# Kernel optimization log

Hardware: AMD Instinct MI355X
Metric: run time of the kernel (lower is better)

Reference implementation:

```python
import jax, jax.numpy as jnp
import numpy as np

NUM_DAYS = 4096
NUM_ATTR = 512
MB = 128  # minibatch_size (sliding-window length)
HID = 500


def setup_inputs() -> dict:
    key = jax.random.key(0)
    kx, k1, kb1, k2, kb2 = jax.random.split(key, 5)
    bound1 = 1.0 / np.sqrt(NUM_ATTR)
    bound2 = 1.0 / np.sqrt(HID)
    return {
        "x": jax.random.normal(kx, (NUM_DAYS, NUM_ATTR), dtype=jnp.float32),
        "W1": jax.random.uniform(k1, (NUM_ATTR, HID), jnp.float32, -bound1, bound1),
        "b1": jax.random.uniform(kb1, (HID,), jnp.float32, -bound1, bound1),
        "W2": jax.random.uniform(k2, (HID, 1), jnp.float32, -bound2, bound2),
        "b2": jax.random.uniform(kb2, (1,), jnp.float32, -bound2, bound2),
    }


def reference(x, W1, b1, W2, b2):
    num_days = x.shape[0]
    num_batches = num_days - MB  # number of sliding windows
    # window gather indices: [num_batches, MB]
    idx = jnp.arange(num_batches)[:, None] + jnp.arange(MB)[None, :]
    xw = x[idx]                                   # [num_batches, MB, num_attr]
    h = jnp.einsum('wma,ah->wmh', xw, W1) + b1    # [num_batches, MB, 500]
    out = jnp.einsum('wmh,ho->wmo', h, W2) + b2   # [num_batches, MB, 1]
    # torch loop cats all windows along dim 0 (first window replaces sentinel)
    return out.reshape(num_batches * MB, 1)
```

## Files before the change

kernel.cpp:

```cpp
#include <hip/hip_runtime.h>

#define NUM_DAYS   4096
#define NUM_ATTR   512
#define MB_WIN     128
#define HID        500
#define NUM_BATCHES (NUM_DAYS - MB_WIN)
#define NUM_Y       (NUM_BATCHES + MB_WIN - 1)
#define OUT_ELEMS   (NUM_BATCHES * MB_WIN)

__global__ __launch_bounds__(64) void k_fold_weights(
    const float* __restrict__ W1, const float* __restrict__ b1,
    const float* __restrict__ W2, const float* __restrict__ b2,
    float* __restrict__ v, float* __restrict__ c) {
    const int b    = blockIdx.x;
    const int lane = threadIdx.x;
    float acc = 0.f;
    if (b < NUM_ATTR) {
        const float* row = W1 + (size_t)b * HID;
        for (int h = lane; h < HID; h += 64) acc += row[h] * W2[h];
    } else {
        for (int h = lane; h < HID; h += 64) acc += b1[h] * W2[h];
    }
    #pragma unroll
    for (int off = 32; off >= 1; off >>= 1) acc += __shfl_down(acc, off, 64);
    if (lane == 0) {
        if (b < NUM_ATTR) v[b] = acc;
        else              *c   = acc + b2[0];
    }
}

__global__ __launch_bounds__(64) void k_day_dot(
    const float* __restrict__ x, const float* __restrict__ v,
    const float* __restrict__ c, float* __restrict__ y) {
    const int d    = blockIdx.x;
    const int lane = threadIdx.x;
    const float4* xr = (const float4*)(x + (size_t)d * NUM_ATTR);
    const float4* vr = (const float4*)v;
    float4 a0 = xr[lane];
    float4 a1 = xr[lane + 64];
    float4 v0 = vr[lane];
    float4 v1 = vr[lane + 64];
    float acc = a0.x * v0.x + a0.y * v0.y + a0.z * v0.z + a0.w * v0.w
              + a1.x * v1.x + a1.y * v1.y + a1.z * v1.z + a1.w * v1.w;
    #pragma unroll
    for (int off = 32; off >= 1; off >>= 1) acc += __shfl_down(acc, off, 64);
    if (lane == 0) y[d] = acc + *c;
}

__global__ __launch_bounds__(256) void k_scatter(
    const float* __restrict__ y, float* __restrict__ out) {
    const int i    = blockIdx.x * blockDim.x + threadIdx.x;
    const int base = i << 2;
    const int w    = base >> 7;
    const int m    = base & 127;
    const int d    = w + m;
    float4 r;
    r.x = y[d];
    r.y = y[d + 1];
    r.z = y[d + 2];
    r.w = y[d + 3];
    ((float4*)out)[i] = r;
}

extern "C" void kernel_launch(void* const* d_in, const int* in_sizes, int n_in,
                              void* d_out, int out_size, void* d_ws, size_t ws_size,
                              hipStream_t stream) {
    const float* x  = (const float*)d_in[0];
    const float* W1 = (const float*)d_in[1];
    const float* b1 = (const float*)d_in[2];
    const float* W2 = (const float*)d_in[3];
    const float* b2 = (const float*)d_in[4];
    float* out = (float*)d_out;

    float* ws = (float*)d_ws;
    float* v  = ws;
    float* c  = ws + 512;
    float* y  = ws + 1024;

    k_fold_weights<<<NUM_ATTR + 1, 64, 0, stream>>>(W1, b1, W2, b2, v, c);
    k_day_dot<<<NUM_Y, 64, 0, stream>>>(x, v, c, y);
    k_scatter<<<OUT_ELEMS / 4 / 256, 256, 0, stream>>>(y, out);
}
```

Baseline: 72.14 us.

## Fuse per-day dot product and sliding-window scatter into one kernel

Merges the per-day dot-product kernel and the scatter kernel into a single kernel. Each block handles 16 windows, computes the 143 day values it needs into shared memory, then writes its slice of the output from LDS. This removes one launch and the global round trip for y. In exchange, the overlapping x rows at block boundaries are recomputed, roughly 9x redundant dot-product work.

```diff
diff --git a/kernel.cpp b/kernel.cpp
--- a/kernel.cpp
+++ b/kernel.cpp
@@ -1,12 +1,17 @@
 #include <hip/hip_runtime.h>
 
-#define NUM_DAYS   4096
-#define NUM_ATTR   512
-#define MB_WIN     128
-#define HID        500
+#define NUM_DAYS    4096
+#define NUM_ATTR    512
+#define MB_WIN      128
+#define HID         500
 #define NUM_BATCHES (NUM_DAYS - MB_WIN)
 #define NUM_Y       (NUM_BATCHES + MB_WIN - 1)
 #define OUT_ELEMS   (NUM_BATCHES * MB_WIN)
+
+#define WPB         16
+#define N_BLOCKS    (NUM_BATCHES / WPB)
+#define DAYS_PB     (WPB + MB_WIN - 1)
+#define OUT4_PB     (WPB * MB_WIN / 4)
 
 __global__ __launch_bounds__(64) void k_fold_weights(
     const float* __restrict__ W1, const float* __restrict__ b1,
@@ -29,37 +34,54 @@
     }
 }
 
-__global__ __launch_bounds__(64) void k_day_dot(
+__global__ __launch_bounds__(256) void k_fused_out(
     const float* __restrict__ x, const float* __restrict__ v,
-    const float* __restrict__ c, float* __restrict__ y) {
-    const int d    = blockIdx.x;
-    const int lane = threadIdx.x;
-    const float4* xr = (const float4*)(x + (size_t)d * NUM_ATTR);
-    const float4* vr = (const float4*)v;
-    float4 a0 = xr[lane];
-    float4 a1 = xr[lane + 64];
-    float4 v0 = vr[lane];
-    float4 v1 = vr[lane + 64];
-    float acc = a0.x * v0.x + a0.y * v0.y + a0.z * v0.z + a0.w * v0.w
-              + a1.x * v1.x + a1.y * v1.y + a1.z * v1.z + a1.w * v1.w;
+    const float* __restrict__ c, float* __restrict__ out) {
+    __shared__ float v_lds[NUM_ATTR];
+    __shared__ float y_lds[DAYS_PB];
+    __shared__ float c_s;
+
+    const int tid  = threadIdx.x;
+    const int wave = tid >> 6;
+    const int lane = tid & 63;
+    const int w0   = blockIdx.x * WPB;
+
+    v_lds[tid]       = v[tid];
+    v_lds[tid + 256] = v[tid + 256];
+    if (tid == 0) c_s = *c;
+    __syncthreads();
+
+    const float4* v4 = (const float4*)v_lds;
+    const float4  v0 = v4[lane];
+    const float4  v1 = v4[lane + 64];
+    const float4* x4 = (const float4*)x;
+    for (int t = wave; t < DAYS_PB; t += 4) {
+        const int d = w0 + t;
+        float4 a0 = x4[(size_t)d * 128 + lane];
+        float4 a1 = x4[(size_t)d * 128 + 64 + lane];
+        float acc = a0.x * v0.x + a0.y * v0.y + a0.z * v0.z + a0.w * v0.w
+                  + a1.x * v1.x + a1.y * v1.y + a1.z * v1.z + a1.w * v1.w;
+        #pragma unroll
+        for (int off = 32; off >= 1; off >>= 1) acc += __shfl_down(acc, off, 64);
+        if (lane == 0) y_lds[t] = acc + c_s;
+    }
+    __syncthreads();
+
+    float4* out4 = (float4*)out;
     #pragma unroll
-    for (int off = 32; off >= 1; off >>= 1) acc += __shfl_down(acc, off, 64);
-    if (lane == 0) y[d] = acc + *c;
-}
-
-__global__ __launch_bounds__(256) void k_scatter(
-    const float* __restrict__ y, float* __restrict__ out) {
-    const int i    = blockIdx.x * blockDim.x + threadIdx.x;
-    const int base = i << 2;
-    const int w    = base >> 7;
-    const int m    = base & 127;
-    const int d    = w + m;
-    float4 r;
-    r.x = y[d];
-    r.y = y[d + 1];
-    r.z = y[d + 2];
-    r.w = y[d + 3];
-    ((float4*)out)[i] = r;
+    for (int r = 0; r < OUT4_PB / 256; ++r) {
+        const int j    = tid + r * 256;
+        const int base = j << 2;
+        const int wl   = base >> 7;
+        const int m    = base & 127;
+        const int dl   = wl + m;
+        float4 rr;
+        rr.x = y_lds[dl];
+        rr.y = y_lds[dl + 1];
+        rr.z = y_lds[dl + 2];
+        rr.w = y_lds[dl + 3];
+        out4[(size_t)blockIdx.x * OUT4_PB + j] = rr;
+    }
 }
 
 extern "C" void kernel_launch(void* const* d_in, const int* in_sizes, int n_in,
@@ -75,9 +97,7 @@
     float* ws = (float*)d_ws;
     float* v  = ws;
     float* c  = ws + 512;
-    float* y  = ws + 1024;
 
     k_fold_weights<<<NUM_ATTR + 1, 64, 0, stream>>>(W1, b1, W2, b2, v, c);
-    k_day_dot<<<NUM_Y, 64, 0, stream>>>(x, v, c, y);
-    k_scatter<<<OUT_ELEMS / 4 / 256, 256, 0, stream>>>(y, out);
+    k_fused_out<<<N_BLOCKS, 256, 0, stream>>>(x, v, c, out);
 }
```

After: 87.79 us. 21.7% more time.
